# Kernel optimization log

Hardware: AMD Instinct MI355X
Metric: run time of the kernel (lower is better)

Reference implementation:

```python
import math
import jax, jax.numpy as jnp
import numpy as np

TAU = 1.0
EPS = 1e-6


def _make_projection(m, d, seed=0):
    # FAVOR+ projection: stacked orthogonal d x d blocks (QR of gaussian),
    # rows rescaled by norms of gaussian rows (scaling=0 in the torch code).
    rng = np.random.default_rng(seed)
    blocks = []
    nb_full = m // d
    for _ in range(nb_full):
        q, _ = np.linalg.qr(rng.standard_normal((d, d)))
        blocks.append(q.T)
    rem = m - nb_full * d
    if rem > 0:
        q, _ = np.linalg.qr(rng.standard_normal((d, d)))
        blocks.append(q.T[:rem])
    mat = np.vstack(blocks)
    mult = np.linalg.norm(rng.standard_normal((m, d)), axis=1)
    return jnp.asarray((mult[:, None] * mat).astype(np.float32))


def setup_inputs() -> dict:
    B, N, H, D, d, m = 16, 4096, 8, 64, 64, 128
    key = jax.random.key(0)
    k1, k2, k3 = jax.random.split(key, 3)
    return {
        "x": jax.random.normal(k1, (B, N, H, D), jnp.float32),
        "node_vec1": jax.random.normal(k2, (B, N, H, d), jnp.float32),
        "node_vec2": jax.random.normal(k3, (B, N, H, d), jnp.float32),
        "proj": _make_projection(m, d),
    }


def _feature_map(data, proj, is_query):
    # data: [B,N,H,d], proj: [m,d]
    d = data.shape[-1]
    data = data * (1.0 / jnp.sqrt(jnp.sqrt(jnp.float32(d))))
    ratio = 1.0 / jnp.sqrt(jnp.float32(proj.shape[0]))
    data_dash = jnp.einsum('bnhd,md->bnhm', data, proj)
    diag = 0.5 * jnp.sum(data * data, axis=-1, keepdims=True)  # [B,N,H,1]
    if is_query:
        mx = jnp.max(data_dash, axis=-1, keepdims=True)
    else:
        # max over feature dim then over sequence/node dim (axis 1)
        mx = jnp.max(jnp.max(data_dash, axis=-1, keepdims=True), axis=1, keepdims=True)
    return ratio * (jnp.exp(data_dash - diag - mx) + EPS)


def reference(x, node_vec1, node_vec2, proj):
    inv_sqrt_tau = 1.0 / math.sqrt(TAU)
    v1p = _feature_map(node_vec1 * inv_sqrt_tau, proj, True)   # [B,N,H,m]
    v2p = _feature_map(node_vec2 * inv_sqrt_tau, proj, False)  # [B,N,H,m]
    # linear (kernelized) attention: O(N) in sequence length
    v2x = jnp.einsum('bnhm,bnhd->bhmd', v2p, x)                 # [B,H,m,D]
    out1 = jnp.einsum('bnhm,bhmd->bnhd', v1p, v2x)              # [B,N,H,D]
    v2_sum = jnp.sum(v2p, axis=1)                               # [B,H,m]
    out2 = jnp.einsum('bnhm,bhm->bnh', v1p, v2_sum)[..., None]  # [B,N,H,1]
    return (out1 / out2, v1p, v2p)
```

## Files before the change

kernel.cpp:

```cpp
#include <hip/hip_runtime.h>
#include <math.h>

constexpr int CN = 4096, CHH = 8, CD = 64, CM = 128;
constexpr int V1P_OFF = 16 * 4096 * 8 * 64;
constexpr int V2P_OFF = V1P_OFF + 16 * 4096 * 8 * 128;
constexpr float KSCALE = 0.35355339059327373f;
constexpr float KRATIO = 0.08838834764831843f;
constexpr float KEPS   = 1e-6f;

typedef __attribute__((ext_vector_type(8))) short bf16x8;
typedef __attribute__((ext_vector_type(4))) float f32x4;

__device__ __forceinline__ float dot4(float4 a, float4 b) {
  return fmaf(a.x, b.x, fmaf(a.y, b.y, fmaf(a.z, b.z, a.w * b.w)));
}
__device__ __forceinline__ float4 scl4(float4 a, float s) {
  return make_float4(a.x * s, a.y * s, a.z * s, a.w * s);
}
__device__ __forceinline__ short bhi(float f) {
  return (short)(__float_as_uint(f) >> 16);
}
__device__ __forceinline__ float bf2f(short s) {
  return __uint_as_float(((unsigned)(unsigned short)s) << 16);
}
__device__ __forceinline__ void split8(float4 u, float4 v, bf16x8& hi, bf16x8& lo) {
  float a[8] = {u.x, u.y, u.z, u.w, v.x, v.y, v.z, v.w};
#pragma unroll
  for (int e = 0; e < 8; e++) {
    short h = bhi(a[e]);
    hi[e] = h;
    lo[e] = bhi(a[e] - bf2f(h));
  }
}
__device__ __forceinline__ void split8a(const float* a, bf16x8& hi, bf16x8& lo) {
#pragma unroll
  for (int e = 0; e < 8; e++) {
    short h = bhi(a[e]);
    hi[e] = h;
    lo[e] = bhi(a[e] - bf2f(h));
  }
}

#define MFMA_B16(A, B, C) __builtin_amdgcn_mfma_f32_16x16x32_bf16(A, B, C, 0, 0, 0)

#define LOAD_BFRAGS(proj, lm, ko)                                   \
  bf16x8 Bh0[8], Bl0[8], Bh1[8], Bl1[8];                            \
  _Pragma("unroll")                                                 \
  for (int t = 0; t < 8; t++) {                                     \
    const float* pb = (proj) + (t * 16 + (lm)) * 64 + (ko);         \
    float4 p0 = *(const float4*)(pb);                               \
    float4 p1 = *(const float4*)(pb + 4);                           \
    float4 p2 = *(const float4*)(pb + 32);                          \
    float4 p3 = *(const float4*)(pb + 36);                          \
    split8(p0, p1, Bh0[t], Bl0[t]);                                 \
    split8(p2, p3, Bh1[t], Bl1[t]);                                 \
  }

#define PROJ_MFMA(acc, t)                                           \
  do {                                                              \
    acc = MFMA_B16(Ah0, Bh0[t], acc);                               \
    acc = MFMA_B16(Ah1, Bh1[t], acc);                               \
    acc = MFMA_B16(Al0, Bh0[t], acc);                               \
    acc = MFMA_B16(Al1, Bh1[t], acc);                               \
    acc = MFMA_B16(Ah0, Bl0[t], acc);                               \
    acc = MFMA_B16(Ah1, Bl1[t], acc);                               \
  } while (0)

__global__ __launch_bounds__(256) void kp_stat(
    const float* __restrict__ inp, const float* __restrict__ proj,
    float* __restrict__ outmax) {
  const int l = threadIdx.x & 63, w = threadIdx.x >> 6;
  const int lm = l & 15, lk = l >> 4, ko = lk * 8;
  LOAD_BFRAGS(proj, lm, ko);
  const int bh = blockIdx.x >> 3, ch = blockIdx.x & 7;
  const int b = bh >> 3, h = bh & 7;
  float bmax = -1e30f;
  for (int s = 0; s < 8; s++) {
    const int nb = ch * 512 + w * 128 + s * 16;
    const size_t rA = (size_t)((b * CN + nb + lm) * CHH + h);
    const float* pa = inp + rA * 64 + ko;
    float4 a0 = scl4(*(const float4*)(pa), KSCALE);
    float4 a1 = scl4(*(const float4*)(pa + 4), KSCALE);
    float4 a2 = scl4(*(const float4*)(pa + 32), KSCALE);
    float4 a3 = scl4(*(const float4*)(pa + 36), KSCALE);
    bf16x8 Ah0, Al0, Ah1, Al1;
    split8(a0, a1, Ah0, Al0);
    split8(a2, a3, Ah1, Al1);
    float rm[4] = {-1e30f, -1e30f, -1e30f, -1e30f};
#pragma unroll
    for (int t = 0; t < 8; t++) {
      f32x4 acc = {0.f, 0.f, 0.f, 0.f};
      PROJ_MFMA(acc, t);
#pragma unroll
      for (int r = 0; r < 4; r++) rm[r] = fmaxf(rm[r], acc[r]);
    }
    bmax = fmaxf(fmaxf(bmax, fmaxf(rm[0], rm[1])), fmaxf(rm[2], rm[3]));
  }
  float v = bmax;
#pragma unroll
  for (int d = 1; d < 64; d <<= 1) v = fmaxf(v, __shfl_xor(v, d));
  __shared__ float wred[4];
  if (l == 0) wred[w] = v;
  __syncthreads();
  if (threadIdx.x == 0)
    outmax[blockIdx.x] = fmaxf(fmaxf(wred[0], wred[1]), fmaxf(wred[2], wred[3]));
}

__global__ __launch_bounds__(256) void kp_emit(
    const float* __restrict__ inp, const float* __restrict__ proj,
    const float* __restrict__ partmax, float* __restrict__ outp) {
  const int l = threadIdx.x & 63, w = threadIdx.x >> 6;
  const int lm = l & 15, lk = l >> 4, ko = lk * 8;
  LOAD_BFRAGS(proj, lm, ko);
  const int bh = blockIdx.x >> 3, ch = blockIdx.x & 7;
  const int b = bh >> 3, h = bh & 7;
  float whm = -1e30f;
#pragma unroll
  for (int c = 0; c < 8; c++) whm = fmaxf(whm, partmax[bh * 8 + c]);
  for (int s = 0; s < 8; s++) {
    const int nb = ch * 512 + w * 128 + s * 16;
    const size_t rA = (size_t)((b * CN + nb + lm) * CHH + h);
    const float* pa = inp + rA * 64 + ko;
    float4 a0 = scl4(*(const float4*)(pa), KSCALE);
    float4 a1 = scl4(*(const float4*)(pa + 4), KSCALE);
    float4 a2 = scl4(*(const float4*)(pa + 32), KSCALE);
    float4 a3 = scl4(*(const float4*)(pa + 36), KSCALE);
    bf16x8 Ah0, Al0, Ah1, Al1;
    split8(a0, a1, Ah0, Al0);
    split8(a2, a3, Ah1, Al1);
    float dp = dot4(a0, a0) + dot4(a1, a1) + dot4(a2, a2) + dot4(a3, a3);
    dp += __shfl_xor(dp, 16);
    dp += __shfl_xor(dp, 32);
    float c[4];
    size_t obase[4];
#pragma unroll
    for (int r = 0; r < 4; r++) {
      const float dg = __shfl(dp, lk * 4 + r);
      const size_t rr = (size_t)((b * CN + nb + lk * 4 + r) * CHH + h);
      c[r] = -(0.5f * dg + whm);
      obase[r] = rr * CM + lm;
    }
#pragma unroll
    for (int t = 0; t < 8; t++) {
      f32x4 acc = {0.f, 0.f, 0.f, 0.f};
      PROJ_MFMA(acc, t);
#pragma unroll
      for (int r = 0; r < 4; r++)
        outp[obase[r] + t * 16] = KRATIO * (__expf(acc[r] + c[r]) + KEPS);
    }
  }
}

__global__ __launch_bounds__(256) void k3m(
    const float* __restrict__ v2p, const float* __restrict__ x,
    float* __restrict__ part, float* __restrict__ vsumpart) {
  const int l = threadIdx.x & 63, w = threadIdx.x >> 6;
  const int lm = l & 15, lk = l >> 4;
  const int bh = blockIdx.x >> 3, ch = blockIdx.x & 7;
  const int b = bh >> 3, h = bh & 7;
  const int jt0 = w * 2;
  f32x4 acc[2][4];
#pragma unroll
  for (int jj = 0; jj < 2; jj++)
#pragma unroll
    for (int dt = 0; dt < 4; dt++) acc[jj][dt] = (f32x4){0.f, 0.f, 0.f, 0.f};
  float vs0 = 0.f, vs1 = 0.f;
  for (int t = 0; t < 16; t++) {
    const int n0 = ch * 512 + t * 32 + lk * 8;
    bf16x8 Ah[2], Al[2];
#pragma unroll
    for (int jj = 0; jj < 2; jj++) {
      float af[8];
#pragma unroll
      for (int e = 0; e < 8; e++)
        af[e] = v2p[(size_t)((b * CN + n0 + e) * CHH + h) * CM + (jt0 + jj) * 16 + lm];
      split8a(af, Ah[jj], Al[jj]);
      float p = 0.f;
#pragma unroll
      for (int e = 0; e < 8; e++) p += af[e];
      if (jj == 0) vs0 += p; else vs1 += p;
    }
#pragma unroll
    for (int dt = 0; dt < 4; dt++) {
      float bfv[8];
#pragma unroll
      for (int e = 0; e < 8; e++)
        bfv[e] = x[(size_t)((b * CN + n0 + e) * CHH + h) * CD + dt * 16 + lm];
      bf16x8 Bh, Bl;
      split8a(bfv, Bh, Bl);
#pragma unroll
      for (int jj = 0; jj < 2; jj++) {
        acc[jj][dt] = MFMA_B16(Ah[jj], Bh, acc[jj][dt]);
        acc[jj][dt] = MFMA_B16(Al[jj], Bh, acc[jj][dt]);
        acc[jj][dt] = MFMA_B16(Ah[jj], Bl, acc[jj][dt]);
      }
    }
  }
  const size_t pbase = (size_t)blockIdx.x * 8192;
#pragma unroll
  for (int jj = 0; jj < 2; jj++)
#pragma unroll
    for (int dt = 0; dt < 4; dt++)
#pragma unroll
      for (int r = 0; r < 4; r++)
        part[pbase + ((size_t)(jt0 + jj) * 16 + lk * 4 + r) * 64 + dt * 16 + lm] = acc[jj][dt][r];
  float v0 = vs0, v1 = vs1;
  v0 += __shfl_xor(v0, 16); v0 += __shfl_xor(v0, 32);
  v1 += __shfl_xor(v1, 16); v1 += __shfl_xor(v1, 32);
  if (lk == 0) {
    vsumpart[(size_t)blockIdx.x * 128 + (jt0 + 0) * 16 + lm] = v0;
    vsumpart[(size_t)blockIdx.x * 128 + (jt0 + 1) * 16 + lm] = v1;
  }
}

__global__ void k3b_reduce(const float* __restrict__ part, const float* __restrict__ vsumpart,
                           float* __restrict__ v2x, float* __restrict__ vsum) {
  const int i = blockIdx.x * 256 + threadIdx.x;
  if (i < 1048576) {
    const int bh = i >> 13, r = i & 8191;
    float s = 0.f;
#pragma unroll
    for (int c = 0; c < 8; c++) s += part[(size_t)(bh * 8 + c) * 8192 + r];
    v2x[i] = s;
  } else if (i < 1048576 + 16384) {
    const int k = i - 1048576, bh = k >> 7, j = k & 127;
    float s = 0.f;
#pragma unroll
    for (int c = 0; c < 8; c++) s += vsumpart[(size_t)(bh * 8 + c) * 128 + j];
    vsum[k] = s;
  }
}

__global__ __launch_bounds__(256) void kv1e(
    const float* __restrict__ inp, const float* __restrict__ proj,
    float* __restrict__ outp) {
  const int l = threadIdx.x & 63, w = threadIdx.x >> 6;
  const int lm = l & 15, lk = l >> 4, ko = lk * 8;
  LOAD_BFRAGS(proj, lm, ko);
  const int bh = blockIdx.x >> 3, ch = blockIdx.x & 7;
  const int b = bh >> 3, h = bh & 7;
  for (int s = 0; s < 8; s++) {
    const int nb = ch * 512 + w * 128 + s * 16;
    const size_t rA = (size_t)((b * CN + nb + lm) * CHH + h);
    const float* pa = inp + rA * 64 + ko;
    float4 a0 = scl4(*(const float4*)(pa), KSCALE);
    float4 a1 = scl4(*(const float4*)(pa + 4), KSCALE);
    float4 a2 = scl4(*(const float4*)(pa + 32), KSCALE);
    float4 a3 = scl4(*(const float4*)(pa + 36), KSCALE);
    bf16x8 Ah0, Al0, Ah1, Al1;
    split8(a0, a1, Ah0, Al0);
    split8(a2, a3, Ah1, Al1);
    float dp = dot4(a0, a0) + dot4(a1, a1) + dot4(a2, a2) + dot4(a3, a3);
    dp += __shfl_xor(dp, 16);
    dp += __shfl_xor(dp, 32);
    f32x4 acc8[8];
#pragma unroll
    for (int t = 0; t < 8; t++) {
      f32x4 acc = {0.f, 0.f, 0.f, 0.f};
      PROJ_MFMA(acc, t);
      acc8[t] = acc;
    }
    float rm[4];
#pragma unroll
    for (int r = 0; r < 4; r++) {
      float m = acc8[0][r];
#pragma unroll
      for (int t = 1; t < 8; t++) m = fmaxf(m, acc8[t][r]);
      m = fmaxf(m, __shfl_xor(m, 1));
      m = fmaxf(m, __shfl_xor(m, 2));
      m = fmaxf(m, __shfl_xor(m, 4));
      m = fmaxf(m, __shfl_xor(m, 8));
      rm[r] = m;
    }
    float c[4];
    size_t obase[4];
#pragma unroll
    for (int r = 0; r < 4; r++) {
      const float dg = __shfl(dp, lk * 4 + r);
      const size_t rr = (size_t)((b * CN + nb + lk * 4 + r) * CHH + h);
      c[r] = -(0.5f * dg + rm[r]);
      obase[r] = rr * CM + lm;
    }
#pragma unroll
    for (int t = 0; t < 8; t++) {
#pragma unroll
      for (int r = 0; r < 4; r++)
        outp[obase[r] + t * 16] = KRATIO * (__expf(acc8[t][r] + c[r]) + KEPS);
    }
  }
}

__global__ __launch_bounds__(256) void k4m(
    const float* __restrict__ v1p, const float* __restrict__ v2xg,
    const float* __restrict__ vsumg, float* __restrict__ out0) {
  const int l = threadIdx.x & 63, dt = threadIdx.x >> 6;
  const int lm = l & 15, lk = l >> 4;
  const int bh = blockIdx.x >> 4, ch = blockIdx.x & 15;
  const int b = bh >> 3, h = bh & 7;
  bf16x8 Bh[4], Bl[4];
#pragma unroll
  for (int kc = 0; kc < 4; kc++) {
    float bfv[8];
#pragma unroll
    for (int e = 0; e < 8; e++)
      bfv[e] = v2xg[(size_t)bh * 8192 + (size_t)(kc * 32 + lk * 8 + e) * 64 + dt * 16 + lm];
    split8a(bfv, Bh[kc], Bl[kc]);
  }
  float vsr[4][8];
#pragma unroll
  for (int kc = 0; kc < 4; kc++)
#pragma unroll
    for (int e = 0; e < 8; e++)
      vsr[kc][e] = vsumg[bh * 128 + kc * 32 + lk * 8 + e];
  for (int s = 0; s < 16; s++) {
    const int nb = ch * 256 + s * 16;
    const float* pa = v1p + (size_t)((b * CN + nb + lm) * CHH + h) * CM;
    bf16x8 Ah[4], Al[4];
    float o2p = 0.f;
#pragma unroll
    for (int kc = 0; kc < 4; kc++) {
      float4 u = *(const float4*)(pa + kc * 32 + lk * 8);
      float4 v = *(const float4*)(pa + kc * 32 + lk * 8 + 4);
      split8(u, v, Ah[kc], Al[kc]);
      o2p += u.x * vsr[kc][0] + u.y * vsr[kc][1] + u.z * vsr[kc][2] + u.w * vsr[kc][3]
           + v.x * vsr[kc][4] + v.y * vsr[kc][5] + v.z * vsr[kc][6] + v.w * vsr[kc][7];
    }
    o2p += __shfl_xor(o2p, 16);
    o2p += __shfl_xor(o2p, 32);
    f32x4 acc = {0.f, 0.f, 0.f, 0.f};
#pragma unroll
    for (int kc = 0; kc < 4; kc++) {
      acc = MFMA_B16(Ah[kc], Bh[kc], acc);
      acc = MFMA_B16(Al[kc], Bh[kc], acc);
      acc = MFMA_B16(Ah[kc], Bl[kc], acc);
    }
#pragma unroll
    for (int r = 0; r < 4; r++) {
      const float inv = 1.0f / __shfl(o2p, lk * 4 + r);
      out0[(size_t)((b * CN + nb + lk * 4 + r) * CHH + h) * CD + dt * 16 + lm] = acc[r] * inv;
    }
  }
}

extern "C" void kernel_launch(void* const* d_in, const int* in_sizes, int n_in,
                              void* d_out, int out_size, void* d_ws, size_t ws_size,
                              hipStream_t stream) {
  (void)in_sizes; (void)n_in; (void)out_size; (void)ws_size;
  const float* x    = (const float*)d_in[0];
  const float* nv1  = (const float*)d_in[1];
  const float* nv2  = (const float*)d_in[2];
  const float* proj = (const float*)d_in[3];
  float* out  = (float*)d_out;
  float* out0 = out;
  float* v1p  = out + V1P_OFF;
  float* v2p  = out + V2P_OFF;

  float* part     = v1p;
  float* vsumpart = v1p + 8388608;
  float* ws      = (float*)d_ws;
  float* vsum    = ws;
  float* v2x     = ws + 16384;
  float* partmax = ws + 16384 + 1048576;

  kp_stat   <<<dim3(1024), dim3(256), 0, stream>>>(nv2, proj, partmax);
  kp_emit   <<<dim3(1024), dim3(256), 0, stream>>>(nv2, proj, partmax, v2p);
  k3m       <<<dim3(1024), dim3(256), 0, stream>>>(v2p, x, part, vsumpart);
  k3b_reduce<<<dim3(4160), dim3(256), 0, stream>>>(part, vsumpart, v2x, vsum);
  kv1e      <<<dim3(1024), dim3(256), 0, stream>>>(nv1, proj, v1p);
  k4m       <<<dim3(2048), dim3(256), 0, stream>>>(v1p, v2x, vsum, out0);
}
```

Measured before the change: 507.0 us.

## Co-schedule v1 feature map with v2 stat/emit passes in fused launches

The stat and emit kernels for the key feature map become device functions. Two combined kernels each run 1536 blocks: 1024 blocks for one v2 pass plus half of the independent v1 feature-map blocks. This drops one launch and lets v1 work share the GPU with the lighter v2 passes instead of running in its own serial launch. Because v1p is now written before k3m, the k3m partial-sum scratch moves from the v1p buffer into the out0 buffer, which k4m only overwrites later. The cost is a per-block branch and heterogeneous blocks within one grid.

```diff
diff --git a/kernel.cpp b/kernel.cpp
--- a/kernel.cpp
+++ b/kernel.cpp
@@ -66,13 +66,13 @@
     acc = MFMA_B16(Ah1, Bl1[t], acc);                               \
   } while (0)
 
-__global__ __launch_bounds__(256) void kp_stat(
+__device__ __forceinline__ void body_stat(
     const float* __restrict__ inp, const float* __restrict__ proj,
-    float* __restrict__ outmax) {
+    float* __restrict__ outmax, int bid) {
   const int l = threadIdx.x & 63, w = threadIdx.x >> 6;
   const int lm = l & 15, lk = l >> 4, ko = lk * 8;
   LOAD_BFRAGS(proj, lm, ko);
-  const int bh = blockIdx.x >> 3, ch = blockIdx.x & 7;
+  const int bh = bid >> 3, ch = bid & 7;
   const int b = bh >> 3, h = bh & 7;
   float bmax = -1e30f;
   for (int s = 0; s < 8; s++) {
@@ -103,16 +103,16 @@
   if (l == 0) wred[w] = v;
   __syncthreads();
   if (threadIdx.x == 0)
-    outmax[blockIdx.x] = fmaxf(fmaxf(wred[0], wred[1]), fmaxf(wred[2], wred[3]));
-}
-
-__global__ __launch_bounds__(256) void kp_emit(
+    outmax[bid] = fmaxf(fmaxf(wred[0], wred[1]), fmaxf(wred[2], wred[3]));
+}
+
+__device__ __forceinline__ void body_emit(
     const float* __restrict__ inp, const float* __restrict__ proj,
-    const float* __restrict__ partmax, float* __restrict__ outp) {
+    const float* __restrict__ partmax, float* __restrict__ outp, int bid) {
   const int l = threadIdx.x & 63, w = threadIdx.x >> 6;
   const int lm = l & 15, lk = l >> 4, ko = lk * 8;
   LOAD_BFRAGS(proj, lm, ko);
-  const int bh = blockIdx.x >> 3, ch = blockIdx.x & 7;
+  const int bh = bid >> 3, ch = bid & 7;
   const int b = bh >> 3, h = bh & 7;
   float whm = -1e30f;
 #pragma unroll
@@ -151,93 +151,13 @@
   }
 }
 
-__global__ __launch_bounds__(256) void k3m(
-    const float* __restrict__ v2p, const float* __restrict__ x,
-    float* __restrict__ part, float* __restrict__ vsumpart) {
-  const int l = threadIdx.x & 63, w = threadIdx.x >> 6;
-  const int lm = l & 15, lk = l >> 4;
-  const int bh = blockIdx.x >> 3, ch = blockIdx.x & 7;
-  const int b = bh >> 3, h = bh & 7;
-  const int jt0 = w * 2;
-  f32x4 acc[2][4];
-#pragma unroll
-  for (int jj = 0; jj < 2; jj++)
-#pragma unroll
-    for (int dt = 0; dt < 4; dt++) acc[jj][dt] = (f32x4){0.f, 0.f, 0.f, 0.f};
-  float vs0 = 0.f, vs1 = 0.f;
-  for (int t = 0; t < 16; t++) {
-    const int n0 = ch * 512 + t * 32 + lk * 8;
-    bf16x8 Ah[2], Al[2];
-#pragma unroll
-    for (int jj = 0; jj < 2; jj++) {
-      float af[8];
-#pragma unroll
-      for (int e = 0; e < 8; e++)
-        af[e] = v2p[(size_t)((b * CN + n0 + e) * CHH + h) * CM + (jt0 + jj) * 16 + lm];
-      split8a(af, Ah[jj], Al[jj]);
-      float p = 0.f;
-#pragma unroll
-      for (int e = 0; e < 8; e++) p += af[e];
-      if (jj == 0) vs0 += p; else vs1 += p;
-    }
-#pragma unroll
-    for (int dt = 0; dt < 4; dt++) {
-      float bfv[8];
-#pragma unroll
-      for (int e = 0; e < 8; e++)
-        bfv[e] = x[(size_t)((b * CN + n0 + e) * CHH + h) * CD + dt * 16 + lm];
-      bf16x8 Bh, Bl;
-      split8a(bfv, Bh, Bl);
-#pragma unroll
-      for (int jj = 0; jj < 2; jj++) {
-        acc[jj][dt] = MFMA_B16(Ah[jj], Bh, acc[jj][dt]);
-        acc[jj][dt] = MFMA_B16(Al[jj], Bh, acc[jj][dt]);
-        acc[jj][dt] = MFMA_B16(Ah[jj], Bl, acc[jj][dt]);
-      }
-    }
-  }
-  const size_t pbase = (size_t)blockIdx.x * 8192;
-#pragma unroll
-  for (int jj = 0; jj < 2; jj++)
-#pragma unroll
-    for (int dt = 0; dt < 4; dt++)
-#pragma unroll
-      for (int r = 0; r < 4; r++)
-        part[pbase + ((size_t)(jt0 + jj) * 16 + lk * 4 + r) * 64 + dt * 16 + lm] = acc[jj][dt][r];
-  float v0 = vs0, v1 = vs1;
-  v0 += __shfl_xor(v0, 16); v0 += __shfl_xor(v0, 32);
-  v1 += __shfl_xor(v1, 16); v1 += __shfl_xor(v1, 32);
-  if (lk == 0) {
-    vsumpart[(size_t)blockIdx.x * 128 + (jt0 + 0) * 16 + lm] = v0;
-    vsumpart[(size_t)blockIdx.x * 128 + (jt0 + 1) * 16 + lm] = v1;
-  }
-}
-
-__global__ void k3b_reduce(const float* __restrict__ part, const float* __restrict__ vsumpart,
-                           float* __restrict__ v2x, float* __restrict__ vsum) {
-  const int i = blockIdx.x * 256 + threadIdx.x;
-  if (i < 1048576) {
-    const int bh = i >> 13, r = i & 8191;
-    float s = 0.f;
-#pragma unroll
-    for (int c = 0; c < 8; c++) s += part[(size_t)(bh * 8 + c) * 8192 + r];
-    v2x[i] = s;
-  } else if (i < 1048576 + 16384) {
-    const int k = i - 1048576, bh = k >> 7, j = k & 127;
-    float s = 0.f;
-#pragma unroll
-    for (int c = 0; c < 8; c++) s += vsumpart[(size_t)(bh * 8 + c) * 128 + j];
-    vsum[k] = s;
-  }
-}
-
-__global__ __launch_bounds__(256) void kv1e(
+__device__ __forceinline__ void body_v1e(
     const float* __restrict__ inp, const float* __restrict__ proj,
-    float* __restrict__ outp) {
+    float* __restrict__ outp, int bid) {
   const int l = threadIdx.x & 63, w = threadIdx.x >> 6;
   const int lm = l & 15, lk = l >> 4, ko = lk * 8;
   LOAD_BFRAGS(proj, lm, ko);
-  const int bh = blockIdx.x >> 3, ch = blockIdx.x & 7;
+  const int bh = bid >> 3, ch = bid & 7;
   const int b = bh >> 3, h = bh & 7;
   for (int s = 0; s < 8; s++) {
     const int nb = ch * 512 + w * 128 + s * 16;
@@ -290,6 +210,102 @@
   }
 }
 
+__global__ __launch_bounds__(256) void kfused1(
+    const float* __restrict__ nv2, const float* __restrict__ nv1,
+    const float* __restrict__ proj, float* __restrict__ partmax,
+    float* __restrict__ v1p) {
+  if (blockIdx.x < 1024) body_stat(nv2, proj, partmax, blockIdx.x);
+  else                   body_v1e(nv1, proj, v1p, blockIdx.x - 1024);
+}
+
+__global__ __launch_bounds__(256) void kfused2(
+    const float* __restrict__ nv2, const float* __restrict__ nv1,
+    const float* __restrict__ proj, const float* __restrict__ partmax,
+    float* __restrict__ v2p, float* __restrict__ v1p) {
+  if (blockIdx.x < 1024) body_emit(nv2, proj, partmax, v2p, blockIdx.x);
+  else                   body_v1e(nv1, proj, v1p, blockIdx.x - 512);
+}
+
+__global__ __launch_bounds__(256) void k3m(
+    const float* __restrict__ v2p, const float* __restrict__ x,
+    float* __restrict__ part, float* __restrict__ vsumpart) {
+  const int l = threadIdx.x & 63, w = threadIdx.x >> 6;
+  const int lm = l & 15, lk = l >> 4;
+  const int bh = blockIdx.x >> 3, ch = blockIdx.x & 7;
+  const int b = bh >> 3, h = bh & 7;
+  const int jt0 = w * 2;
+  f32x4 acc[2][4];
+#pragma unroll
+  for (int jj = 0; jj < 2; jj++)
+#pragma unroll
+    for (int dt = 0; dt < 4; dt++) acc[jj][dt] = (f32x4){0.f, 0.f, 0.f, 0.f};
+  float vs0 = 0.f, vs1 = 0.f;
+  for (int t = 0; t < 16; t++) {
+    const int n0 = ch * 512 + t * 32 + lk * 8;
+    bf16x8 Ah[2], Al[2];
+#pragma unroll
+    for (int jj = 0; jj < 2; jj++) {
+      float af[8];
+#pragma unroll
+      for (int e = 0; e < 8; e++)
+        af[e] = v2p[(size_t)((b * CN + n0 + e) * CHH + h) * CM + (jt0 + jj) * 16 + lm];
+      split8a(af, Ah[jj], Al[jj]);
+      float p = 0.f;
+#pragma unroll
+      for (int e = 0; e < 8; e++) p += af[e];
+      if (jj == 0) vs0 += p; else vs1 += p;
+    }
+#pragma unroll
+    for (int dt = 0; dt < 4; dt++) {
+      float bfv[8];
+#pragma unroll
+      for (int e = 0; e < 8; e++)
+        bfv[e] = x[(size_t)((b * CN + n0 + e) * CHH + h) * CD + dt * 16 + lm];
+      bf16x8 Bh, Bl;
+      split8a(bfv, Bh, Bl);
+#pragma unroll
+      for (int jj = 0; jj < 2; jj++) {
+        acc[jj][dt] = MFMA_B16(Ah[jj], Bh, acc[jj][dt]);
+        acc[jj][dt] = MFMA_B16(Al[jj], Bh, acc[jj][dt]);
+        acc[jj][dt] = MFMA_B16(Ah[jj], Bl, acc[jj][dt]);
+      }
+    }
+  }
+  const size_t pbase = (size_t)blockIdx.x * 8192;
+#pragma unroll
+  for (int jj = 0; jj < 2; jj++)
+#pragma unroll
+    for (int dt = 0; dt < 4; dt++)
+#pragma unroll
+      for (int r = 0; r < 4; r++)
+        part[pbase + ((size_t)(jt0 + jj) * 16 + lk * 4 + r) * 64 + dt * 16 + lm] = acc[jj][dt][r];
+  float v0 = vs0, v1 = vs1;
+  v0 += __shfl_xor(v0, 16); v0 += __shfl_xor(v0, 32);
+  v1 += __shfl_xor(v1, 16); v1 += __shfl_xor(v1, 32);
+  if (lk == 0) {
+    vsumpart[(size_t)blockIdx.x * 128 + (jt0 + 0) * 16 + lm] = v0;
+    vsumpart[(size_t)blockIdx.x * 128 + (jt0 + 1) * 16 + lm] = v1;
+  }
+}
+
+__global__ void k3b_reduce(const float* __restrict__ part, const float* __restrict__ vsumpart,
+                           float* __restrict__ v2x, float* __restrict__ vsum) {
+  const int i = blockIdx.x * 256 + threadIdx.x;
+  if (i < 1048576) {
+    const int bh = i >> 13, r = i & 8191;
+    float s = 0.f;
+#pragma unroll
+    for (int c = 0; c < 8; c++) s += part[(size_t)(bh * 8 + c) * 8192 + r];
+    v2x[i] = s;
+  } else if (i < 1048576 + 16384) {
+    const int k = i - 1048576, bh = k >> 7, j = k & 127;
+    float s = 0.f;
+#pragma unroll
+    for (int c = 0; c < 8; c++) s += vsumpart[(size_t)(bh * 8 + c) * 128 + j];
+    vsum[k] = s;
+  }
+}
+
 __global__ __launch_bounds__(256) void k4m(
     const float* __restrict__ v1p, const float* __restrict__ v2xg,
     const float* __restrict__ vsumg, float* __restrict__ out0) {
@@ -355,17 +371,16 @@
   float* v1p  = out + V1P_OFF;
   float* v2p  = out + V2P_OFF;
 
-  float* part     = v1p;
-  float* vsumpart = v1p + 8388608;
+  float* part     = out0;
+  float* vsumpart = out0 + 8388608;
   float* ws      = (float*)d_ws;
   float* vsum    = ws;
   float* v2x     = ws + 16384;
   float* partmax = ws + 16384 + 1048576;
 
-  kp_stat   <<<dim3(1024), dim3(256), 0, stream>>>(nv2, proj, partmax);
-  kp_emit   <<<dim3(1024), dim3(256), 0, stream>>>(nv2, proj, partmax, v2p);
+  kfused1   <<<dim3(1536), dim3(256), 0, stream>>>(nv2, nv1, proj, partmax, v1p);
+  kfused2   <<<dim3(1536), dim3(256), 0, stream>>>(nv2, nv1, proj, partmax, v2p, v1p);
   k3m       <<<dim3(1024), dim3(256), 0, stream>>>(v2p, x, part, vsumpart);
   k3b_reduce<<<dim3(4160), dim3(256), 0, stream>>>(part, vsumpart, v2x, vsum);
-  kv1e      <<<dim3(1024), dim3(256), 0, stream>>>(nv1, proj, v1p);
   k4m       <<<dim3(2048), dim3(256), 0, stream>>>(v1p, v2x, vsum, out0);
 }
```

New measurement: 516.6 us. Within noise of the previous version (+1.9%).
